# Kernel optimization log

Measured on AMD Instinct MI355X. Metric: run time of the kernel, lower is better.

Reference implementation:

```python
import jax, jax.numpy as jnp
import numpy as np

HEAD_DIM = 64

def setup_inputs() -> dict:
    key = jax.random.key(0)
    k1, k2, k3, k4, k5 = jax.random.split(key, 5)
    T, B, E = 2048, 4, 1024
    KD = 64  # kdim
    x = jax.random.normal(k1, (T, B, E), dtype=jnp.float32)
    in_proj_weight = jax.random.normal(k2, (3 * KD, HEAD_DIM), dtype=jnp.float32) * (1.0 / np.sqrt(HEAD_DIM))
    in_proj_bias = jnp.zeros((3 * KD,), dtype=jnp.float32)
    out_w = jax.random.normal(k4, (HEAD_DIM, KD), dtype=jnp.float32) * (1.0 / np.sqrt(KD))
    out_b = jnp.zeros((HEAD_DIM,), dtype=jnp.float32)
    return {"x": x, "in_proj_weight": in_proj_weight, "in_proj_bias": in_proj_bias,
            "out_w": out_w, "out_b": out_b}

def reference(x, in_proj_weight, in_proj_bias, out_w, out_b):
    # x: [T, B, E] with E = H * HEAD_DIM (qkv_same self-attention path)
    T, B, E = x.shape
    H = E // HEAD_DIM
    KD = in_proj_weight.shape[0] // 3
    scaling = HEAD_DIM ** (-0.5)
    # reshape splits embed dim into heads: [T, B*H, 64]
    xh = x.reshape(T, B * H, HEAD_DIM)
    # fused in-projection: [T, B*H, 3*KD], then chunk into q/k/v
    qkv = xh @ in_proj_weight.T + in_proj_bias
    q, k, v = jnp.split(qkv, 3, axis=-1)          # each [T, B*H, KD]
    q = q * scaling
    q = q.transpose(1, 0, 2)                      # [B*H, T, KD]
    k = k.transpose(1, 0, 2)
    v = v.transpose(1, 0, 2)
    scores = jnp.einsum('btd,bsd->bts', q, k)     # [B*H, T, T]
    w = jax.nn.softmax(scores, axis=-1)
    attn = jnp.einsum('bts,bsd->btd', w, v)       # [B*H, T, KD]
    attn = attn.transpose(1, 0, 2).reshape(T, B, H, KD)
    out = attn @ out_w.T + out_b                  # [T, B, H, HEAD_DIM]
    out = out.reshape(T, B, H * HEAD_DIM)         # [T, B, E]
    # averaged attention weights over heads: [B, T, T]
    avg_w = w.reshape(B, H, T, T).sum(axis=1) / H
    return out, avg_w
```

## Files before the change

### kernel.cpp

```cpp
#include <hip/hip_runtime.h>
#include <hip/hip_bf16.h>

#define T_DIM 2048
#define B_DIM 4
#define E_DIM 1024

typedef __bf16 bf16_t;
typedef bf16_t bf16x8 __attribute__((ext_vector_type(8)));
typedef float f32x4 __attribute__((ext_vector_type(4)));
typedef float f32x16 __attribute__((ext_vector_type(16)));

union frag_u { uint4 u; bf16x8 b; };

constexpr float SCALEQ = 0.18033688011112042f;

__device__ __forceinline__ f32x16 mfma32(bf16x8 a, bf16x8 b, f32x16 c) {
  return __builtin_amdgcn_mfma_f32_32x32x16_bf16(a, b, c, 0, 0, 0);
}
__device__ __forceinline__ unsigned packbf(float a, float b) {
  union { bf16_t h[2]; unsigned u; } r;
  r.h[0] = (bf16_t)a; r.h[1] = (bf16_t)b; return r.u;
}
__device__ __forceinline__ void pl32swap(unsigned &x, unsigned &y) {
  asm volatile("v_permlane32_swap_b32 %0, %1" : "+v"(x), "+v"(y));
}
__device__ __forceinline__ float ex2(float x) { return __builtin_amdgcn_exp2f(x); }

template <int O>
__device__ __forceinline__ uint4 mkfrag(const f32x16& A) {
  unsigned X = packbf(A[O + 0], A[O + 1]);
  unsigned Z = packbf(A[O + 2], A[O + 3]);
  unsigned Y = packbf(A[O + 4], A[O + 5]);
  unsigned W = packbf(A[O + 6], A[O + 7]);
  pl32swap(X, Y); pl32swap(Z, W);
  return (uint4){X, Z, Y, W};
}

__global__ __launch_bounds__(256) void qkv_kernel(
    const float* __restrict__ x, const float* __restrict__ W,
    const float* __restrict__ bias,
    bf16_t* __restrict__ Qc, bf16_t* __restrict__ Kc, bf16_t* __restrict__ Vc) {
  __shared__ __align__(16) char xlds[16384];
  __shared__ __align__(16) char wlds[24576];
  __shared__ float bs[192];
  const int tid = threadIdx.x;
  const int bh = blockIdx.x >> 4;
  const int tt = blockIdx.x & 15;
  const int b = bh >> 4, h = bh & 15;
  const int t0 = tt * 128;
  const int wid = tid >> 6, lane = tid & 63;
  const int lq = lane & 31, hi = lane >> 5;

  for (int i = tid; i < 1024; i += 256) {
    int t = i >> 3, oct = i & 7;
    const float* src = x + ((size_t)(t0 + t) * B_DIM + b) * E_DIM + h * 64 + oct * 8;
    float4 f0 = *(const float4*)src;
    float4 f1 = *(const float4*)(src + 4);
    uint4 u;
    u.x = packbf(f0.x, f0.y); u.y = packbf(f0.z, f0.w);
    u.z = packbf(f1.x, f1.y); u.w = packbf(f1.z, f1.w);
    *(uint4*)(xlds + oct * 2048 + t * 16) = u;
  }
  for (int i = tid; i < 1536; i += 256) {
    int r = i >> 3, oct = i & 7;
    const float* src = W + r * 64 + oct * 8;
    float4 f0 = *(const float4*)src;
    float4 f1 = *(const float4*)(src + 4);
    uint4 u;
    u.x = packbf(f0.x, f0.y); u.y = packbf(f0.z, f0.w);
    u.z = packbf(f1.x, f1.y); u.w = packbf(f1.z, f1.w);
    *(uint4*)(wlds + oct * 3072 + r * 16) = u;
  }
  if (tid < 192) bs[tid] = bias[tid];
  __syncthreads();

  frag_u bx[4];
  #pragma unroll
  for (int s = 0; s < 4; ++s)
    bx[s].u = *(const uint4*)(xlds + (s * 2 + hi) * 2048 + (wid * 32 + lq) * 16);

  f32x16 acc[6];
  #pragma unroll
  for (int mt = 0; mt < 6; ++mt)
    #pragma unroll
    for (int r = 0; r < 16; ++r) acc[mt][r] = 0.f;

  #pragma unroll
  for (int mt = 0; mt < 6; ++mt) {
    #pragma unroll
    for (int s = 0; s < 4; ++s) {
      frag_u aw;
      aw.u = *(const uint4*)(wlds + (s * 2 + hi) * 3072 + (mt * 32 + lq) * 16);
      acc[mt] = mfma32(aw.b, bx[s].b, acc[mt]);
    }
  }

  const size_t tb = ((size_t)bh * 32 + (t0 >> 6) + (wid >> 1)) * 4096;
  const int trow = (wid & 1) * 32 + lq;

  #pragma unroll
  for (int mt = 0; mt < 6; ++mt) {
    #pragma unroll
    for (int g = 0; g < 4; ++g) {
      int rbase = mt * 32 + 8 * g + 4 * hi;
      float4 bq = *(const float4*)&bs[rbase];
      float v0 = acc[mt][4 * g + 0] + bq.x;
      float v1 = acc[mt][4 * g + 1] + bq.y;
      float v2 = acc[mt][4 * g + 2] + bq.z;
      float v3 = acc[mt][4 * g + 3] + bq.w;
      if (mt < 2) {
        union { ushort4 us; unsigned u2[2]; } pk;
        pk.u2[0] = packbf(v0 * SCALEQ, v1 * SCALEQ);
        pk.u2[1] = packbf(v2 * SCALEQ, v3 * SCALEQ);
        int d0 = rbase;
        *(ushort4*)(Qc + tb + (d0 >> 3) * 512 + trow * 8 + (d0 & 7)) = pk.us;
      } else if (mt < 4) {
        union { ushort4 us; unsigned u2[2]; } pk;
        pk.u2[0] = packbf(v0, v1);
        pk.u2[1] = packbf(v2, v3);
        int d0 = rbase - 64;
        *(ushort4*)(Kc + tb + (d0 >> 3) * 512 + trow * 8 + (d0 & 7)) = pk.us;
      } else {
        int d0 = rbase - 128;
        bf16_t* vdst = Vc + tb + (trow >> 3) * 512 + (trow & 7);
        vdst[(size_t)(d0 + 0) * 8] = (bf16_t)v0;
        vdst[(size_t)(d0 + 1) * 8] = (bf16_t)v1;
        vdst[(size_t)(d0 + 2) * 8] = (bf16_t)v2;
        vdst[(size_t)(d0 + 3) * 8] = (bf16_t)v3;
      }
    }
  }
}

__global__ __launch_bounds__(256, 2) void flash_kernel(
    const bf16_t* __restrict__ Qc, const bf16_t* __restrict__ Kc,
    const bf16_t* __restrict__ Vc,
    const float* __restrict__ Wo, const float* __restrict__ bo,
    float* __restrict__ out, float* __restrict__ Lv) {
  const int tid = threadIdx.x;
  const int bh = blockIdx.x & 63;
  const int qb = blockIdx.x >> 6;
  const int b = bh >> 4, h = bh & 15;
  const int wid = tid >> 6, lane = tid & 63;
  const int lq = lane & 31, hi = lane >> 5;
  const int qw = qb * 256 + wid * 64;

  const bf16_t* qtb = Qc + ((size_t)bh * 32 + (qw >> 6)) * 4096;
  frag_u qfA[4], qfB[4];
  #pragma unroll
  for (int s = 0; s < 4; ++s) {
    qfA[s].u = *(const uint4*)(qtb + (s * 2 + hi) * 512 + lq * 8);
    qfB[s].u = *(const uint4*)(qtb + (s * 2 + hi) * 512 + (32 + lq) * 8);
  }

  frag_u ones;
  #pragma unroll
  for (int j = 0; j < 8; ++j) ones.b[j] = (bf16_t)1.0f;

  f32x16 zc;
  #pragma unroll
  for (int i = 0; i < 16; ++i) zc[i] = 0.f;

  f32x16 oA0, oA1, oB0, oB1, lmfA, lmfB;
  #pragma unroll
  for (int i = 0; i < 16; ++i) {
    oA0[i] = 0.f; oA1[i] = 0.f; oB0[i] = 0.f; oB1[i] = 0.f;
    lmfA[i] = 0.f; lmfB[i] = 0.f;
  }

  const bf16_t* kbh = Kc + (size_t)bh * 131072;
  const bf16_t* vbh = Vc + (size_t)bh * 131072;

  for (int t = 0; t < 32; ++t) {
    const bf16_t* kt = kbh + (size_t)t * 4096;
    const bf16_t* vt = vbh + (size_t)t * 4096;

    bf16x8 k0[4], k1[4], v0[4], v1[4];
    #pragma unroll
    for (int s = 0; s < 4; ++s) {
      frag_u f0, f1, g0, g1;
      f0.u = *(const uint4*)(kt + (s * 2 + hi) * 512 + lq * 8);
      f1.u = *(const uint4*)(kt + (s * 2 + hi) * 512 + (32 + lq) * 8);
      g0.u = *(const uint4*)(vt + (s * 2 + hi) * 512 + lq * 8);
      g1.u = *(const uint4*)(vt + (s * 2 + hi) * 512 + (32 + lq) * 8);
      k0[s] = f0.b; k1[s] = f1.b; v0[s] = g0.b; v1[s] = g1.b;
    }

    f32x16 aA0, aA1, aB0, aB1;
    __builtin_amdgcn_s_setprio(1);
    aA0 = mfma32(k0[0], qfA[0].b, zc);
    aA1 = mfma32(k1[0], qfA[0].b, zc);
    aB0 = mfma32(k0[0], qfB[0].b, zc);
    aB1 = mfma32(k1[0], qfB[0].b, zc);
    #pragma unroll
    for (int s = 1; s < 4; ++s) {
      aA0 = mfma32(k0[s], qfA[s].b, aA0);
      aA1 = mfma32(k1[s], qfA[s].b, aA1);
      aB0 = mfma32(k0[s], qfB[s].b, aB0);
      aB1 = mfma32(k1[s], qfB[s].b, aB1);
    }
    __builtin_amdgcn_s_setprio(0);

    #pragma unroll
    for (int i = 0; i < 16; ++i) {
      aA0[i] = ex2(aA0[i]); aA1[i] = ex2(aA1[i]);
      aB0[i] = ex2(aB0[i]); aB1[i] = ex2(aB1[i]);
    }

    frag_u pA0, pA1, pA2, pA3, pB0, pB1, pB2, pB3;
    pA0.u = mkfrag<0>(aA0); pA1.u = mkfrag<8>(aA0);
    pA2.u = mkfrag<0>(aA1); pA3.u = mkfrag<8>(aA1);
    pB0.u = mkfrag<0>(aB0); pB1.u = mkfrag<8>(aB0);
    pB2.u = mkfrag<0>(aB1); pB3.u = mkfrag<8>(aB1);

    __builtin_amdgcn_s_setprio(1);
    oA0 = mfma32(v0[0], pA0.b, oA0); oA1 = mfma32(v1[0], pA0.b, oA1);
    oB0 = mfma32(v0[0], pB0.b, oB0); oB1 = mfma32(v1[0], pB0.b, oB1);
    oA0 = mfma32(v0[1], pA1.b, oA0); oA1 = mfma32(v1[1], pA1.b, oA1);
    oB0 = mfma32(v0[1], pB1.b, oB0); oB1 = mfma32(v1[1], pB1.b, oB1);
    oA0 = mfma32(v0[2], pA2.b, oA0); oA1 = mfma32(v1[2], pA2.b, oA1);
    oB0 = mfma32(v0[2], pB2.b, oB0); oB1 = mfma32(v1[2], pB2.b, oB1);
    oA0 = mfma32(v0[3], pA3.b, oA0); oA1 = mfma32(v1[3], pA3.b, oA1);
    oB0 = mfma32(v0[3], pB3.b, oB0); oB1 = mfma32(v1[3], pB3.b, oB1);
    lmfA = mfma32(ones.b, pA0.b, lmfA); lmfA = mfma32(ones.b, pA1.b, lmfA);
    lmfA = mfma32(ones.b, pA2.b, lmfA); lmfA = mfma32(ones.b, pA3.b, lmfA);
    lmfB = mfma32(ones.b, pB0.b, lmfB); lmfB = mfma32(ones.b, pB1.b, lmfB);
    lmfB = mfma32(ones.b, pB2.b, lmfB); lmfB = mfma32(ones.b, pB3.b, lmfB);
    __builtin_amdgcn_s_setprio(0);
  }

  float ltA = lmfA[0], ltB = lmfB[0];
  float iA = 1.f / ltA, iB = 1.f / ltB;
  #pragma unroll
  for (int i = 0; i < 16; ++i) { oA0[i] *= iA; oA1[i] *= iA; oB0[i] *= iB; oB1[i] *= iB; }

  frag_u fA[4], fB[4];
  fA[0].u = mkfrag<0>(oA0); fA[1].u = mkfrag<8>(oA0);
  fA[2].u = mkfrag<0>(oA1); fA[3].u = mkfrag<8>(oA1);
  fB[0].u = mkfrag<0>(oB0); fB[1].u = mkfrag<8>(oB0);
  fB[2].u = mkfrag<0>(oB1); fB[3].u = mkfrag<8>(oB1);

  f32x16 cA0, cA1, cB0, cB1;
  #pragma unroll
  for (int i = 0; i < 16; ++i) { cA0[i] = 0.f; cA1[i] = 0.f; cB0[i] = 0.f; cB1[i] = 0.f; }
  #pragma unroll
  for (int s = 0; s < 4; ++s) {
    frag_u w0, w1;
    {
      const float* ws0 = Wo + lq * 64 + (s * 2 + hi) * 8;
      float4 a = *(const float4*)ws0;
      float4 c = *(const float4*)(ws0 + 4);
      w0.u = (uint4){packbf(a.x, a.y), packbf(a.z, a.w),
                     packbf(c.x, c.y), packbf(c.z, c.w)};
      const float* ws1 = Wo + (32 + lq) * 64 + (s * 2 + hi) * 8;
      float4 d = *(const float4*)ws1;
      float4 e = *(const float4*)(ws1 + 4);
      w1.u = (uint4){packbf(d.x, d.y), packbf(d.z, d.w),
                     packbf(e.x, e.y), packbf(e.z, e.w)};
    }
    cA0 = mfma32(fA[s].b, w0.b, cA0);
    cA1 = mfma32(fA[s].b, w1.b, cA1);
    cB0 = mfma32(fB[s].b, w0.b, cB0);
    cB1 = mfma32(fB[s].b, w1.b, cB1);
  }
  float bo0 = bo[lq], bo1 = bo[32 + lq];
  #pragma unroll
  for (int r = 0; r < 16; ++r) {
    int trA = qw + (r & 3) + 8 * (r >> 2) + 4 * hi;
    int trB = trA + 32;
    out[((size_t)trA * B_DIM + b) * E_DIM + h * 64 + lq]      = cA0[r] + bo0;
    out[((size_t)trA * B_DIM + b) * E_DIM + h * 64 + 32 + lq] = cA1[r] + bo1;
    out[((size_t)trB * B_DIM + b) * E_DIM + h * 64 + lq]      = cB0[r] + bo0;
    out[((size_t)trB * B_DIM + b) * E_DIM + h * 64 + 32 + lq] = cB1[r] + bo1;
  }
  if (lane < 32) {
    Lv[(size_t)bh * T_DIM + qw + lq] = ltA;
    Lv[(size_t)bh * T_DIM + qw + 32 + lq] = ltB;
  }
}

__global__ __launch_bounds__(512, 2) void avgw_kernel(
    const bf16_t* __restrict__ Qc, const bf16_t* __restrict__ Kc,
    const float* __restrict__ Lv, float* __restrict__ avgw) {
  __shared__ float lw[16][128];
  const int tid = threadIdx.x;
  const int bid = ((blockIdx.x & 7) << 7) | (blockIdx.x >> 3);
  const int b = bid >> 8, tq = (bid >> 4) & 15, sq = bid & 15;
  const int t0 = tq * 128, s0 = sq * 128;
  const int wid = tid >> 6, lane = tid & 63;
  const int lq = lane & 31, hi = lane >> 5;
  const int wr = wid >> 2, wc = wid & 3;

  for (int i = tid; i < 2048; i += 512) {
    int h = i >> 7, tt = i & 127;
    size_t idx = ((size_t)(b * 16 + h)) * T_DIM + t0 + tt;
    lw[h][tt] = 1.0f / (16.0f * Lv[idx]);
  }
  __syncthreads();

  f32x16 zc;
  #pragma unroll
  for (int r = 0; r < 16; ++r) zc[r] = 0.f;

  f32x16 sacc[2];
  #pragma unroll
  for (int i = 0; i < 2; ++i)
    #pragma unroll
    for (int r = 0; r < 16; ++r) sacc[i][r] = 0.f;

  const int krow = (wc & 1) * 32 + lq;

  for (int h = 0; h < 16; ++h) {
    const int bh = b * 16 + h;
    const bf16_t* qh = Qc + ((size_t)bh * 32 + (t0 >> 6) + wr) * 4096;
    const bf16_t* kh = Kc + ((size_t)bh * 32 + (s0 >> 6) + (wc >> 1)) * 4096;

    frag_u aq[2][4], ak[4];
    #pragma unroll
    for (int s = 0; s < 4; ++s) {
      ak[s].u = *(const uint4*)(kh + (s * 2 + hi) * 512 + krow * 8);
      aq[0][s].u = *(const uint4*)(qh + (s * 2 + hi) * 512 + lq * 8);
      aq[1][s].u = *(const uint4*)(qh + (s * 2 + hi) * 512 + (32 + lq) * 8);
    }

    #pragma unroll
    for (int i = 0; i < 2; ++i) {
      __builtin_amdgcn_s_setprio(1);
      f32x16 c = mfma32(aq[i][0].b, ak[0].b, zc);
      #pragma unroll
      for (int s = 1; s < 4; ++s) c = mfma32(aq[i][s].b, ak[s].b, c);
      __builtin_amdgcn_s_setprio(0);
      #pragma unroll
      for (int g = 0; g < 4; ++g) {
        f32x4 l4 = *(const f32x4*)&lw[h][wr * 64 + i * 32 + 8 * g + 4 * hi];
        #pragma unroll
        for (int e = 0; e < 4; ++e)
          sacc[i][4 * g + e] += ex2(c[4 * g + e]) * l4[e];
      }
    }
  }

  #pragma unroll
  for (int i = 0; i < 2; ++i)
    #pragma unroll
    for (int r = 0; r < 16; ++r) {
      int trow = t0 + wr * 64 + i * 32 + (r & 3) + ((r >> 2) << 3) + (hi << 2);
      int scol = s0 + wc * 32 + lq;
      avgw[((size_t)b * T_DIM + trow) * T_DIM + scol] = sacc[i][r];
    }
}

extern "C" void kernel_launch(void* const* d_in, const int* in_sizes, int n_in,
                              void* d_out, int out_size, void* d_ws, size_t ws_size,
                              hipStream_t stream) {
  const float* x    = (const float*)d_in[0];
  const float* W    = (const float*)d_in[1];
  const float* bias = (const float*)d_in[2];
  const float* Wo   = (const float*)d_in[3];
  const float* bo   = (const float*)d_in[4];
  float* out  = (float*)d_out;
  float* avgw = out + (size_t)T_DIM * B_DIM * E_DIM;

  char* ws = (char*)d_ws;
  bf16_t* Qc = (bf16_t*)(ws);
  bf16_t* Kc = (bf16_t*)(ws + (16u << 20));
  bf16_t* Vc = (bf16_t*)(ws + (32u << 20));
  float*  Lv = (float*)(ws + (48u << 20));

  qkv_kernel<<<dim3(1024), dim3(256), 0, stream>>>(x, W, bias, Qc, Kc, Vc);
  flash_kernel<<<dim3(512), dim3(256), 0, stream>>>(Qc, Kc, Vc, Wo, bo, out, Lv);
  avgw_kernel<<<dim3(1024), dim3(512), 0, stream>>>(Qc, Kc, Lv, avgw);
}
```

Before: 181.7 us.

## Double-buffer Q/K tiles in LDS for avgw, drop ones-MFMA row sums in flash

```diff
diff --git a/kernel.cpp b/kernel.cpp
--- a/kernel.cpp
+++ b/kernel.cpp
@@ -24,7 +24,20 @@
 __device__ __forceinline__ void pl32swap(unsigned &x, unsigned &y) {
   asm volatile("v_permlane32_swap_b32 %0, %1" : "+v"(x), "+v"(y));
 }
+__device__ __forceinline__ void gload16(const void* g, void* l) {
+  __builtin_amdgcn_global_load_lds((const __attribute__((address_space(1))) void*)g,
+                                   (__attribute__((address_space(3))) void*)l, 16, 0, 0);
+}
 __device__ __forceinline__ float ex2(float x) { return __builtin_amdgcn_exp2f(x); }
+
+#define VMCNT4 do { asm volatile("s_waitcnt vmcnt(4)" ::: "memory"); \
+                    __builtin_amdgcn_sched_barrier(0); } while (0)
+#define VMCNT0 do { asm volatile("s_waitcnt vmcnt(0)" ::: "memory"); \
+                    __builtin_amdgcn_sched_barrier(0); } while (0)
+#define LGKM0  do { asm volatile("s_waitcnt lgkmcnt(0)" ::: "memory"); \
+                    __builtin_amdgcn_sched_barrier(0); } while (0)
+#define SBAR   do { __builtin_amdgcn_s_barrier(); \
+                    __builtin_amdgcn_sched_barrier(0); } while (0)
 
 template <int O>
 __device__ __forceinline__ uint4 mkfrag(const f32x16& A) {
@@ -34,6 +47,15 @@
   unsigned W = packbf(A[O + 6], A[O + 7]);
   pl32swap(X, Y); pl32swap(Z, W);
   return (uint4){X, Z, Y, W};
+}
+
+__device__ __forceinline__ float tree16(const f32x16& v) {
+  float a0 = v[0] + v[1],   a1 = v[2] + v[3];
+  float a2 = v[4] + v[5],   a3 = v[6] + v[7];
+  float a4 = v[8] + v[9],   a5 = v[10] + v[11];
+  float a6 = v[12] + v[13], a7 = v[14] + v[15];
+  float b0 = a0 + a1, b1 = a2 + a3, b2 = a4 + a5, b3 = a6 + a7;
+  return (b0 + b1) + (b2 + b3);
 }
 
 __global__ __launch_bounds__(256) void qkv_kernel(
@@ -144,6 +166,7 @@
   const int wid = tid >> 6, lane = tid & 63;
   const int lq = lane & 31, hi = lane >> 5;
   const int qw = qb * 256 + wid * 64;
+  const int rot = ((wid * 8) + ((qb & 1) * 4)) & 31;
 
   const bf16_t* qtb = Qc + ((size_t)bh * 32 + (qw >> 6)) * 4096;
   frag_u qfA[4], qfB[4];
@@ -153,25 +176,20 @@
     qfB[s].u = *(const uint4*)(qtb + (s * 2 + hi) * 512 + (32 + lq) * 8);
   }
 
-  frag_u ones;
-  #pragma unroll
-  for (int j = 0; j < 8; ++j) ones.b[j] = (bf16_t)1.0f;
-
   f32x16 zc;
   #pragma unroll
   for (int i = 0; i < 16; ++i) zc[i] = 0.f;
 
-  f32x16 oA0, oA1, oB0, oB1, lmfA, lmfB;
-  #pragma unroll
-  for (int i = 0; i < 16; ++i) {
-    oA0[i] = 0.f; oA1[i] = 0.f; oB0[i] = 0.f; oB1[i] = 0.f;
-    lmfA[i] = 0.f; lmfB[i] = 0.f;
-  }
+  f32x16 oA0, oA1, oB0, oB1;
+  #pragma unroll
+  for (int i = 0; i < 16; ++i) { oA0[i] = 0.f; oA1[i] = 0.f; oB0[i] = 0.f; oB1[i] = 0.f; }
+  float lAacc = 0.f, lBacc = 0.f;
 
   const bf16_t* kbh = Kc + (size_t)bh * 131072;
   const bf16_t* vbh = Vc + (size_t)bh * 131072;
 
-  for (int t = 0; t < 32; ++t) {
+  for (int ti = 0; ti < 32; ++ti) {
+    const int t = (ti + rot) & 31;
     const bf16_t* kt = kbh + (size_t)t * 4096;
     const bf16_t* vt = vbh + (size_t)t * 4096;
 
@@ -206,6 +224,8 @@
       aA0[i] = ex2(aA0[i]); aA1[i] = ex2(aA1[i]);
       aB0[i] = ex2(aB0[i]); aB1[i] = ex2(aB1[i]);
     }
+    lAacc += tree16(aA0 + aA1);
+    lBacc += tree16(aB0 + aB1);
 
     frag_u pA0, pA1, pA2, pA3, pB0, pB1, pB2, pB3;
     pA0.u = mkfrag<0>(aA0); pA1.u = mkfrag<8>(aA0);
@@ -222,14 +242,11 @@
     oB0 = mfma32(v0[2], pB2.b, oB0); oB1 = mfma32(v1[2], pB2.b, oB1);
     oA0 = mfma32(v0[3], pA3.b, oA0); oA1 = mfma32(v1[3], pA3.b, oA1);
     oB0 = mfma32(v0[3], pB3.b, oB0); oB1 = mfma32(v1[3], pB3.b, oB1);
-    lmfA = mfma32(ones.b, pA0.b, lmfA); lmfA = mfma32(ones.b, pA1.b, lmfA);
-    lmfA = mfma32(ones.b, pA2.b, lmfA); lmfA = mfma32(ones.b, pA3.b, lmfA);
-    lmfB = mfma32(ones.b, pB0.b, lmfB); lmfB = mfma32(ones.b, pB1.b, lmfB);
-    lmfB = mfma32(ones.b, pB2.b, lmfB); lmfB = mfma32(ones.b, pB3.b, lmfB);
     __builtin_amdgcn_s_setprio(0);
   }
 
-  float ltA = lmfA[0], ltB = lmfB[0];
+  float ltA = lAacc + __shfl_xor(lAacc, 32);
+  float ltB = lBacc + __shfl_xor(lBacc, 32);
   float iA = 1.f / ltA, iB = 1.f / ltB;
   #pragma unroll
   for (int i = 0; i < 16; ++i) { oA0[i] *= iA; oA1[i] *= iA; oB0[i] *= iB; oB1[i] *= iB; }
@@ -282,6 +299,8 @@
 __global__ __launch_bounds__(512, 2) void avgw_kernel(
     const bf16_t* __restrict__ Qc, const bf16_t* __restrict__ Kc,
     const float* __restrict__ Lv, float* __restrict__ avgw) {
+  __shared__ __align__(16) char qlds[2][16384];
+  __shared__ __align__(16) char klds[2][16384];
   __shared__ float lw[16][128];
   const int tid = threadIdx.x;
   const int bid = ((blockIdx.x & 7) << 7) | (blockIdx.x >> 3);
@@ -296,7 +315,17 @@
     size_t idx = ((size_t)(b * 16 + h)) * T_DIM + t0 + tt;
     lw[h][tt] = 1.0f / (16.0f * Lv[idx]);
   }
-  __syncthreads();
+
+  auto stage = [&](int buf, int h) {
+    int bh = b * 16 + h;
+    const bf16_t* qt = Qc + ((size_t)bh * 32 + (t0 >> 6)) * 4096;
+    const bf16_t* kt = Kc + ((size_t)bh * 32 + (s0 >> 6)) * 4096;
+    #pragma unroll
+    for (int j = 0; j < 2; ++j) {
+      gload16(qt + wid * 1024 + j * 512 + lane * 8, qlds[buf] + wid * 2048 + j * 1024);
+      gload16(kt + wid * 1024 + j * 512 + lane * 8, klds[buf] + wid * 2048 + j * 1024);
+    }
+  };
 
   f32x16 zc;
   #pragma unroll
@@ -308,20 +337,28 @@
     #pragma unroll
     for (int r = 0; r < 16; ++r) sacc[i][r] = 0.f;
 
-  const int krow = (wc & 1) * 32 + lq;
+  stage(0, 0); stage(1, 1);
+  VMCNT4; LGKM0;
+  SBAR;
 
   for (int h = 0; h < 16; ++h) {
-    const int bh = b * 16 + h;
-    const bf16_t* qh = Qc + ((size_t)bh * 32 + (t0 >> 6) + wr) * 4096;
-    const bf16_t* kh = Kc + ((size_t)bh * 32 + (s0 >> 6) + (wc >> 1)) * 4096;
+    const char* qb = qlds[h & 1];
+    const char* kb = klds[h & 1];
 
     frag_u aq[2][4], ak[4];
     #pragma unroll
     for (int s = 0; s < 4; ++s) {
-      ak[s].u = *(const uint4*)(kh + (s * 2 + hi) * 512 + krow * 8);
-      aq[0][s].u = *(const uint4*)(qh + (s * 2 + hi) * 512 + lq * 8);
-      aq[1][s].u = *(const uint4*)(qh + (s * 2 + hi) * 512 + (32 + lq) * 8);
-    }
+      int rk = wc * 32 + lq;
+      ak[s].u = *(const uint4*)(kb + (rk >> 6) * 8192 + (s * 2 + hi) * 1024 + (rk & 63) * 16);
+      #pragma unroll
+      for (int i = 0; i < 2; ++i) {
+        int rq = wr * 64 + i * 32 + lq;
+        aq[i][s].u = *(const uint4*)(qb + (rq >> 6) * 8192 + (s * 2 + hi) * 1024 + (rq & 63) * 16);
+      }
+    }
+    LGKM0;
+    SBAR;
+    if (h + 2 < 16) stage(h & 1, h + 2);
 
     #pragma unroll
     for (int i = 0; i < 2; ++i) {
@@ -338,6 +375,9 @@
           sacc[i][4 * g + e] += ex2(c[4 * g + e]) * l4[e];
       }
     }
+
+    if (h < 14) { VMCNT4; } else { VMCNT0; }
+    SBAR;
   }
 
   #pragma unroll
```

New measurement: 176.2 us. 1.03x faster.
